# Kernel optimization log

Hardware: AMD Instinct MI355X
Metric: run time of the kernel (lower is better)

Reference implementation:

```python
import jax, jax.numpy as jnp
import numpy as np

ROPE_BASE = 10000.0
NEG_INF = -1e30

def _apply_rope(x):
    # x: [B, H, T, D]; interleaved-pair RoPE (torchtune style), positions along axis -2.
    B, H, T, D = x.shape
    inv_freq = 1.0 / (ROPE_BASE ** (jnp.arange(0, D, 2, dtype=jnp.float32) / D))  # [D/2]
    ang = jnp.arange(T, dtype=jnp.float32)[:, None] * inv_freq[None, :]           # [T, D/2]
    cos, sin = jnp.cos(ang), jnp.sin(ang)
    x1, x2 = x[..., 0::2], x[..., 1::2]                                           # [B,H,T,D/2]
    rot = jnp.stack([x1 * cos - x2 * sin, x1 * sin + x2 * cos], axis=-1)          # [B,H,T,D/2,2]
    return rot.reshape(B, H, T, D).astype(x.dtype)

def setup_inputs() -> dict:
    key = jax.random.key(0)
    ks = jax.random.split(key, 5)
    B, T, C = 2, 2048, 1024
    s = 1.0 / np.sqrt(C)
    return {
        "x":  jax.random.normal(ks[0], (B, T, C), jnp.float32),
        "Wq": jax.random.normal(ks[1], (C, C), jnp.float32) * s,
        "bq": jnp.zeros((C,), jnp.float32),
        "Wk": jax.random.normal(ks[2], (C, C), jnp.float32) * s,
        "bk": jnp.zeros((C,), jnp.float32),
        "Wv": jax.random.normal(ks[3], (C, C), jnp.float32) * s,
        "bv": jnp.zeros((C,), jnp.float32),
        "Wo": jax.random.normal(ks[4], (C, C), jnp.float32) * s,
        "bo": jnp.zeros((C,), jnp.float32),
    }

def reference(x, Wq, bq, Wk, bk, Wv, bv, Wo, bo):
    B, T, C = x.shape
    H = 16
    D = C // H
    # QKV projections (torch Linear: x @ W.T + b), split heads -> [B, H, T, D]
    def proj(W, b):
        return (jnp.einsum('btc,oc->bto', x, W) + b).reshape(B, T, H, D).transpose(0, 2, 1, 3)
    q = _apply_rope(proj(Wq, bq))
    k = _apply_rope(proj(Wk, bk))
    v = proj(Wv, bv)
    # Causal scaled dot-product attention
    scale = 1.0 / jnp.sqrt(jnp.asarray(D, x.dtype))
    scores = jnp.einsum('bhqd,bhkd->bhqk', q, k) * scale                          # [B,H,T,T]
    causal = jnp.tril(jnp.ones((T, T), dtype=bool))
    scores = jnp.where(causal, scores, NEG_INF)
    probs = jax.nn.softmax(scores, axis=-1)
    y = jnp.einsum('bhqk,bhkd->bhqd', probs, v)                                   # [B,H,T,D]
    y = y.transpose(0, 2, 1, 3).reshape(B, T, C)
    # Output projection (dropout is identity in eval mode)
    return jnp.einsum('btc,oc->bto', y, Wo) + bo
```

## Files before the change

### kernel.cpp

```cpp
#include <hip/hip_runtime.h>

#define BB 2
#define TT 2048
#define CC 1024
#define HH 16
#define DD 64
#define KDIM 1024
#define MROWS (BB*TT)

typedef __attribute__((ext_vector_type(8))) short  frag_b16;
typedef __attribute__((ext_vector_type(4))) float  f32x4;
typedef __attribute__((ext_vector_type(4))) unsigned short us4;
typedef __attribute__((ext_vector_type(8))) unsigned short us8;
typedef __attribute__((ext_vector_type(4))) _Float16 f16x4;
typedef __attribute__((ext_vector_type(8))) _Float16 f16x8;

#define EXP2F(x) __builtin_amdgcn_exp2f(x)

__device__ __forceinline__ unsigned short f2bf(float f) {
    unsigned int u = __builtin_bit_cast(unsigned int, f);
    u += 0x7FFFu + ((u >> 16) & 1u);
    return (unsigned short)(u >> 16);
}

__device__ __forceinline__ void gl_lds16(const void* g, void* l) {
    __builtin_amdgcn_global_load_lds(
        (const __attribute__((address_space(1))) unsigned int*)g,
        (__attribute__((address_space(3))) unsigned int*)l, 16, 0, 0);
}

__global__ __launch_bounds__(256) void cvt_all(
        const float* __restrict__ x,  const float* __restrict__ w0,
        const float* __restrict__ w1, const float* __restrict__ w2,
        const float* __restrict__ w3, unsigned short* __restrict__ dst) {
    const size_t NX = (size_t)MROWS * CC;
    const size_t NW = (size_t)CC * CC;
    size_t i = ((size_t)blockIdx.x * 256 + threadIdx.x) * 4;
    const float* src; size_t off;
    if (i < NX) { src = x; off = i; }
    else {
        size_t j = i - NX;
        int t = (int)(j >> 20);
        src = (t == 0) ? w0 : (t == 1) ? w1 : (t == 2) ? w2 : w3;
        off = j & (NW - 1);
    }
    float4 f = *reinterpret_cast<const float4*>(src + off);
    us4 o;
    o.x = f2bf(f.x); o.y = f2bf(f.y); o.z = f2bf(f.z); o.w = f2bf(f.w);
    *reinterpret_cast<us4*>(dst + i) = o;
}

__global__ __launch_bounds__(256, 3) void qkv_gemm_rope(
        const unsigned short* __restrict__ X,
        const unsigned short* __restrict__ Wq,
        const unsigned short* __restrict__ Wk,
        const unsigned short* __restrict__ Wv,
        const float* __restrict__ bq, const float* __restrict__ bk,
        const float* __restrict__ bv,
        unsigned short* __restrict__ Qo,
        unsigned short* __restrict__ Ko,
        _Float16* __restrict__ VTo)
{
    const int z = blockIdx.z;
    const unsigned short* W = (z == 0) ? Wq : (z == 1) ? Wk : Wv;
    const float* bias = (z == 0) ? bq : (z == 1) ? bk : bv;

    const int tid = threadIdx.x;
    const int wave = tid >> 6;
    const int lane = tid & 63;
    const int l16 = lane & 15;
    const int quad = lane >> 4;

    const int bx = blockIdx.x * 128;
    const int by = blockIdx.y * 128;
    const int row0 = bx + (wave >> 1) * 64;
    const int col0 = by + (wave & 1) * 64;

    __shared__ __align__(16) char smem[36864];
    unsigned short (*Xa)[32] = (unsigned short(*)[32])smem;
    unsigned short (*Wb)[32] = (unsigned short(*)[32])(smem + 8192);
    _Float16 (*Vl)[64][72] = (_Float16(*)[64][72])smem;

    f32x4 acc[4][4] = {};

    const int c0 = tid, c1 = tid + 256;
    const int r0s = c0 >> 2, o0s = (c0 & 3) * 8;
    const int r1s = c1 >> 2, o1s = (c1 & 3) * 8;

    for (int kk = 0; kk < KDIM; kk += 32) {
        gl_lds16(X + (size_t)(bx + r0s) * KDIM + kk + o0s, (unsigned short*)Xa + c0 * 8);
        gl_lds16(X + (size_t)(bx + r1s) * KDIM + kk + o1s, (unsigned short*)Xa + c1 * 8);
        gl_lds16(W + (size_t)(by + r0s) * KDIM + kk + o0s, (unsigned short*)Wb + c0 * 8);
        gl_lds16(W + (size_t)(by + r1s) * KDIM + kk + o1s, (unsigned short*)Wb + c1 * 8);
        __syncthreads();

        frag_b16 a[4], b[4];
#pragma unroll
        for (int r = 0; r < 4; ++r)
            a[r] = *reinterpret_cast<const frag_b16*>(
                &Xa[(wave >> 1) * 64 + r * 16 + l16][quad * 8]);
#pragma unroll
        for (int c = 0; c < 4; ++c)
            b[c] = *reinterpret_cast<const frag_b16*>(
                &Wb[(wave & 1) * 64 + c * 16 + l16][quad * 8]);
#pragma unroll
        for (int r = 0; r < 4; ++r)
#pragma unroll
            for (int c = 0; c < 4; ++c)
                acc[r][c] = __builtin_amdgcn_mfma_f32_16x16x32_bf16(a[r], b[c], acc[r][c], 0, 0, 0);
        __syncthreads();
    }

    if (z == 2) {
#pragma unroll
        for (int r = 0; r < 4; ++r)
#pragma unroll
            for (int c = 0; c < 4; ++c) {
                f16x4 pk;
#pragma unroll
                for (int g = 0; g < 4; ++g)
                    pk[g] = (_Float16)(acc[r][c][g] + bias[col0 + c * 16 + l16]);
                *reinterpret_cast<f16x4*>(&Vl[wave][c * 16 + l16][r * 16 + quad * 4]) = pk;
            }
        const int b_ = row0 >> 11;
        const int t_base = row0 & (TT - 1);
        const int h = col0 >> 6;
        const int dl = lane >> 3;
        const int t8 = (lane & 7) * 8;
        __builtin_amdgcn_s_waitcnt(0);
#pragma unroll
        for (int i = 0; i < 8; ++i) {
            int d = i * 8 + dl;
            f16x8 v = *reinterpret_cast<const f16x8*>(&Vl[wave][d][t8]);
            *reinterpret_cast<f16x8*>(
                &VTo[((size_t)(b_ * HH + h) * DD + d) * TT + t_base + t8]) = v;
        }
    } else {
        const float qsc = (z == 0) ? 0.180336888f : 1.0f;
        unsigned short* dst = (z == 0) ? Qo : Ko;
        const int b_ = row0 >> 11;
        const int tq0 = (row0 & (TT - 1)) + quad * 4;
#pragma unroll
        for (int c = 0; c < 4; ++c) {
            const int o = col0 + c * 16 + l16;
            const int h = o >> 6, d = o & (DD - 1);
            const float inv = __expf(-(float)(d & ~1) * (9.210340371976184f / (float)DD));
            float cs0, sn0, cs1, sn1, cs16, sn16;
            __sincosf((float)tq0 * inv, &sn0, &cs0);
            __sincosf(inv, &sn1, &cs1);
            __sincosf(16.f * inv, &sn16, &cs16);
            float cr = cs0, sr = sn0;
#pragma unroll
            for (int r = 0; r < 4; ++r) {
                float cg = cr, sg = sr;
#pragma unroll
                for (int g = 0; g < 4; ++g) {
                    int n = row0 + r * 16 + quad * 4 + g;
                    int t = n & (TT - 1);
                    float v = acc[r][c][g] + bias[o];
                    float pv = __shfl_xor(v, 1);
                    float outv = (d & 1) ? (pv * sg + v * cg) : (v * cg - pv * sg);
                    dst[((size_t)(b_ * HH + h) * TT + t) * DD + d] = f2bf(outv * qsc);
                    float cn = cg * cs1 - sg * sn1;
                    sg = sg * cs1 + cg * sn1;
                    cg = cn;
                }
                float crn = cr * cs16 - sr * sn16;
                sr = sr * cs16 + cr * sn16;
                cr = crn;
            }
        }
    }
}

__global__ __launch_bounds__(256, 2) void attn(
        const unsigned short* __restrict__ Q,
        const unsigned short* __restrict__ K,
        const _Float16* __restrict__ VT,
        unsigned short* __restrict__ Y)
{
    const int b1d = blockIdx.x;
    const int bh = (b1d & 7) * 4 + ((b1d >> 3) & 3);
    const int pair = b1d >> 5;
    const int tid = threadIdx.x;
    const int w = tid >> 6;
    const int lane = tid & 63;
    const int l16 = lane & 15;
    const int quad = lane >> 4;

    const unsigned short* Qp = Q + (size_t)bh * TT * DD;
    const unsigned short* Kp = K + (size_t)bh * TT * DD;
    const _Float16* Vp = VT + (size_t)bh * DD * TT;

    __shared__ unsigned short Kl[2][128][64];
    __shared__ _Float16 Vl[2][64][128];
    __shared__ unsigned short Ylds[4][16][72];

    const int sw = (l16 & 7);
    const int b_ = bh >> 4, h = bh & (HH - 1);

#pragma unroll 1
    for (int seg = 0; seg < 2; ++seg) {
        const int qblk = seg ? (31 - pair) : pair;
        const int q0 = qblk * 64;
        const int q = q0 + w * 16 + l16;

        frag_b16 bq[2];
#pragma unroll
        for (int dk = 0; dk < 2; ++dk)
            bq[dk] = *reinterpret_cast<const frag_b16*>(
                Qp + (size_t)q * DD + dk * 32 + quad * 8);

        f32x4 yacc[4] = {};
        float m = -INFINITY, l = 0.f;

        const int ntiles = (qblk >> 1) + 1;

#pragma unroll
        for (int i = 0; i < 4; ++i) {
            int n = tid + 256 * i;
            int kr = n >> 3,  kc = ((n & 7)  ^ (kr & 7)) * 8;
            int vr = n >> 4,  vc = ((n & 15) ^ (vr & 7)) * 8;
            gl_lds16(Kp + (size_t)kr * DD + kc, (unsigned short*)&Kl[0][0][0] + n * 8);
            gl_lds16(Vp + (size_t)vr * TT + vc, (_Float16*)&Vl[0][0][0] + n * 8);
        }

#pragma unroll 1
        for (int it = 0; it < ntiles; ++it) {
            __syncthreads();
            const int bsel = it & 1;
            if (it + 1 < ntiles) {
                const int jn = (it + 1) * 128;
                const int bn = bsel ^ 1;
#pragma unroll
                for (int i = 0; i < 4; ++i) {
                    int n = tid + 256 * i;
                    int kr = n >> 3,  kc = ((n & 7)  ^ (kr & 7)) * 8;
                    int vr = n >> 4,  vc = ((n & 15) ^ (vr & 7)) * 8;
                    gl_lds16(Kp + (size_t)(jn + kr) * DD + kc,
                             (unsigned short*)&Kl[bn][0][0] + n * 8);
                    gl_lds16(Vp + (size_t)vr * TT + jn + vc,
                             (_Float16*)&Vl[bn][0][0] + n * 8);
                }
            }
            const int j0 = it * 128;

            f32x4 s[8];
#pragma unroll
            for (int mt = 0; mt < 8; ++mt) {
                frag_b16 ak0 = *reinterpret_cast<const frag_b16*>(
                    &Kl[bsel][mt * 16 + l16][(quad ^ sw) * 8]);
                frag_b16 ak1 = *reinterpret_cast<const frag_b16*>(
                    &Kl[bsel][mt * 16 + l16][((4 + quad) ^ sw) * 8]);
                f32x4 t = {};
                t = __builtin_amdgcn_mfma_f32_16x16x32_bf16(ak0, bq[0], t, 0, 0, 0);
                t = __builtin_amdgcn_mfma_f32_16x16x32_bf16(ak1, bq[1], t, 0, 0, 0);
                s[mt] = t;
            }

            float nm = -INFINITY;
            if (it == ntiles - 1) {
#pragma unroll
                for (int mt = 0; mt < 8; ++mt)
#pragma unroll
                    for (int g = 0; g < 4; ++g) {
                        int key = j0 + mt * 16 + quad * 4 + g;
                        float v = s[mt][g];
                        if (key > q) v = -1e30f;
                        s[mt][g] = v;
                        nm = fmaxf(nm, v);
                    }
            } else {
#pragma unroll
                for (int mt = 0; mt < 8; ++mt)
#pragma unroll
                    for (int g = 0; g < 4; ++g)
                        nm = fmaxf(nm, s[mt][g]);
            }
            nm = fmaxf(nm, __shfl_xor(nm, 16));
            nm = fmaxf(nm, __shfl_xor(nm, 32));

            float mn = fmaxf(m, nm);
            float alpha = EXP2F(m - mn);
            m = mn;

            float rs = 0.f;
            f16x4 pb[8];
#pragma unroll
            for (int mt = 0; mt < 8; ++mt)
#pragma unroll
                for (int g = 0; g < 4; ++g) {
                    float e = EXP2F(s[mt][g] - m);
                    pb[mt][g] = (_Float16)e;
                    rs += e;
                }
            rs += __shfl_xor(rs, 16);
            rs += __shfl_xor(rs, 32);
            l = l * alpha + rs;

#pragma unroll
            for (int dt = 0; dt < 4; ++dt) {
                f32x4 ya = yacc[dt];
#pragma unroll
                for (int g = 0; g < 4; ++g) ya[g] *= alpha;
#pragma unroll
                for (int kt = 0; kt < 8; ++kt) {
                    int colp = (kt * 2 + (quad >> 1)) ^ sw;
                    f16x4 av = *reinterpret_cast<const f16x4*>(
                        &Vl[bsel][dt * 16 + l16][colp * 8 + (quad & 1) * 4]);
                    ya = __builtin_amdgcn_mfma_f32_16x16x16f16(av, pb[kt], ya, 0, 0, 0);
                }
                yacc[dt] = ya;
            }
        }

        __syncthreads();

        float rl = 1.f / l;
#pragma unroll
        for (int dt = 0; dt < 4; ++dt)
#pragma unroll
            for (int g = 0; g < 4; ++g)
                Ylds[w][l16][dt * 16 + quad * 4 + g] = f2bf(yacc[dt][g] * rl);

#pragma unroll
        for (int i = 0; i < 2; ++i) {
            int idx = i * 64 + lane;
            int r = idx >> 3, c8 = (idx & 7) * 8;
            us8 v = *reinterpret_cast<const us8*>(&Ylds[w][r][c8]);
            *reinterpret_cast<us8*>(
                &Y[(size_t)(b_ * TT + q0 + w * 16 + r) * CC + h * DD + c8]) = v;
        }
    }
}

__global__ __launch_bounds__(256, 2) void out_gemm(
        const unsigned short* __restrict__ Y,
        const unsigned short* __restrict__ Wo,
        const float* __restrict__ bo,
        float* __restrict__ out)
{
    const int tid = threadIdx.x;
    const int wave = tid >> 6;
    const int lane = tid & 63;
    const int l16 = lane & 15;
    const int quad = lane >> 4;

    const int bx = blockIdx.x * 128;
    const int by = blockIdx.y * 128;
    const int row0 = bx + (wave >> 1) * 64;
    const int col0 = by + (wave & 1) * 64;

    __shared__ unsigned short Xa[128][32];
    __shared__ unsigned short Wb[128][32];

    f32x4 acc[4][4] = {};

    const int c0 = tid, c1 = tid + 256;
    const int r0s = c0 >> 2, o0s = (c0 & 3) * 8;
    const int r1s = c1 >> 2, o1s = (c1 & 3) * 8;

    for (int kk = 0; kk < KDIM; kk += 32) {
        gl_lds16(Y  + (size_t)(bx + r0s) * KDIM + kk + o0s, (unsigned short*)Xa + c0 * 8);
        gl_lds16(Y  + (size_t)(bx + r1s) * KDIM + kk + o1s, (unsigned short*)Xa + c1 * 8);
        gl_lds16(Wo + (size_t)(by + r0s) * KDIM + kk + o0s, (unsigned short*)Wb + c0 * 8);
        gl_lds16(Wo + (size_t)(by + r1s) * KDIM + kk + o1s, (unsigned short*)Wb + c1 * 8);
        __syncthreads();

        frag_b16 a[4], b[4];
#pragma unroll
        for (int r = 0; r < 4; ++r)
            a[r] = *reinterpret_cast<const frag_b16*>(
                &Xa[(wave >> 1) * 64 + r * 16 + l16][quad * 8]);
#pragma unroll
        for (int c = 0; c < 4; ++c)
            b[c] = *reinterpret_cast<const frag_b16*>(
                &Wb[(wave & 1) * 64 + c * 16 + l16][quad * 8]);
#pragma unroll
        for (int r = 0; r < 4; ++r)
#pragma unroll
            for (int c = 0; c < 4; ++c)
                acc[r][c] = __builtin_amdgcn_mfma_f32_16x16x32_bf16(a[r], b[c], acc[r][c], 0, 0, 0);
        __syncthreads();
    }

#pragma unroll
    for (int r = 0; r < 4; ++r)
#pragma unroll
        for (int c = 0; c < 4; ++c)
#pragma unroll
            for (int g = 0; g < 4; ++g) {
                int n = row0 + r * 16 + quad * 4 + g;
                int o = col0 + c * 16 + l16;
                out[(size_t)n * CC + o] = acc[r][c][g] + bo[o];
            }
}

extern "C" void kernel_launch(void* const* d_in, const int* in_sizes, int n_in,
                              void* d_out, int out_size, void* d_ws, size_t ws_size,
                              hipStream_t stream) {
    const float* x  = (const float*)d_in[0];
    const float* Wq = (const float*)d_in[1];
    const float* bq = (const float*)d_in[2];
    const float* Wk = (const float*)d_in[3];
    const float* bk = (const float*)d_in[4];
    const float* Wv = (const float*)d_in[5];
    const float* bv = (const float*)d_in[6];
    const float* Wo = (const float*)d_in[7];
    const float* bo = (const float*)d_in[8];
    float* out = (float*)d_out;

    unsigned short* ws = (unsigned short*)d_ws;
    const size_t NX = (size_t)MROWS * CC;
    const size_t NW = (size_t)CC * CC;
    unsigned short* xb  = ws;
    unsigned short* wqb = xb  + NX;
    unsigned short* wkb = wqb + NW;
    unsigned short* wvb = wkb + NW;
    unsigned short* wob = wvb + NW;
    unsigned short* Qr  = wob + NW;
    unsigned short* Kr  = Qr  + NX;
    _Float16*       VTb = (_Float16*)(Kr + NX);
    unsigned short* Yb  = (unsigned short*)(VTb + NX);

    const size_t NALL = NX + 4 * NW;
    cvt_all<<<dim3((unsigned)(NALL / 1024)), 256, 0, stream>>>(x, Wq, Wk, Wv, Wo, xb);

    qkv_gemm_rope<<<dim3(MROWS / 128, CC / 128, 3), 256, 0, stream>>>(
        xb, wqb, wkb, wvb, bq, bk, bv, Qr, Kr, VTb);

    attn<<<dim3(512), 256, 0, stream>>>(Qr, Kr, VTb, Yb);

    out_gemm<<<dim3(MROWS / 128, CC / 128), 256, 0, stream>>>(Yb, wob, bo, out);
}
```

Before: 183.5 us.

## Process 32 query rows per wave in attention to reuse K/V tiles

```diff
diff --git a/kernel.cpp b/kernel.cpp
--- a/kernel.cpp
+++ b/kernel.cpp
@@ -173,7 +173,7 @@
     }
 }
 
-__global__ __launch_bounds__(256, 2) void attn(
+__global__ __launch_bounds__(256, 1) void attn(
         const unsigned short* __restrict__ Q,
         const unsigned short* __restrict__ K,
         const _Float16* __restrict__ VT,
@@ -194,27 +194,29 @@
 
     __shared__ unsigned short Kl[2][128][64];
     __shared__ _Float16 Vl[2][64][128];
-    __shared__ unsigned short Ylds[4][16][72];
+    __shared__ unsigned short Ylds[4][32][72];
 
     const int sw = (l16 & 7);
     const int b_ = bh >> 4, h = bh & (HH - 1);
 
 #pragma unroll 1
     for (int seg = 0; seg < 2; ++seg) {
-        const int qblk = seg ? (31 - pair) : pair;
-        const int q0 = qblk * 64;
-        const int q = q0 + w * 16 + l16;
-
-        frag_b16 bq[2];
-#pragma unroll
-        for (int dk = 0; dk < 2; ++dk)
-            bq[dk] = *reinterpret_cast<const frag_b16*>(
-                Qp + (size_t)q * DD + dk * 32 + quad * 8);
-
-        f32x4 yacc[4] = {};
-        float m = -INFINITY, l = 0.f;
-
-        const int ntiles = (qblk >> 1) + 1;
+        const int qblk = seg ? (15 - pair) : pair;
+        const int q0 = qblk * 128;
+        const int qw = q0 + w * 32;
+
+        frag_b16 bq[2][2];
+#pragma unroll
+        for (int nt = 0; nt < 2; ++nt)
+#pragma unroll
+            for (int dk = 0; dk < 2; ++dk)
+                bq[nt][dk] = *reinterpret_cast<const frag_b16*>(
+                    Qp + (size_t)(qw + nt * 16 + l16) * DD + dk * 32 + quad * 8);
+
+        f32x4 yacc[2][4] = {};
+        float m[2] = { -INFINITY, -INFINITY }, l[2] = { 0.f, 0.f };
+
+        const int ntiles = qblk + 1;
 
 #pragma unroll
         for (int i = 0; i < 4; ++i) {
@@ -245,91 +247,121 @@
             }
             const int j0 = it * 128;
 
-            f32x4 s[8];
+            f32x4 s[2][8];
 #pragma unroll
             for (int mt = 0; mt < 8; ++mt) {
                 frag_b16 ak0 = *reinterpret_cast<const frag_b16*>(
                     &Kl[bsel][mt * 16 + l16][(quad ^ sw) * 8]);
                 frag_b16 ak1 = *reinterpret_cast<const frag_b16*>(
                     &Kl[bsel][mt * 16 + l16][((4 + quad) ^ sw) * 8]);
-                f32x4 t = {};
-                t = __builtin_amdgcn_mfma_f32_16x16x32_bf16(ak0, bq[0], t, 0, 0, 0);
-                t = __builtin_amdgcn_mfma_f32_16x16x32_bf16(ak1, bq[1], t, 0, 0, 0);
-                s[mt] = t;
-            }
-
-            float nm = -INFINITY;
-            if (it == ntiles - 1) {
+#pragma unroll
+                for (int nt = 0; nt < 2; ++nt) {
+                    f32x4 t = {};
+                    t = __builtin_amdgcn_mfma_f32_16x16x32_bf16(ak0, bq[nt][0], t, 0, 0, 0);
+                    t = __builtin_amdgcn_mfma_f32_16x16x32_bf16(ak1, bq[nt][1], t, 0, 0, 0);
+                    s[nt][mt] = t;
+                }
+            }
+
+            float nm[2] = { -INFINITY, -INFINITY };
+            if (it == qblk) {
+#pragma unroll
+                for (int nt = 0; nt < 2; ++nt) {
+                    const int q = qw + nt * 16 + l16;
+#pragma unroll
+                    for (int mt = 0; mt < 8; ++mt)
+#pragma unroll
+                        for (int g = 0; g < 4; ++g) {
+                            int key = j0 + mt * 16 + quad * 4 + g;
+                            float v = s[nt][mt][g];
+                            if (key > q) v = -1e30f;
+                            s[nt][mt][g] = v;
+                            nm[nt] = fmaxf(nm[nt], v);
+                        }
+                }
+            } else {
+#pragma unroll
+                for (int nt = 0; nt < 2; ++nt)
+#pragma unroll
+                    for (int mt = 0; mt < 8; ++mt)
+#pragma unroll
+                        for (int g = 0; g < 4; ++g)
+                            nm[nt] = fmaxf(nm[nt], s[nt][mt][g]);
+            }
+#pragma unroll
+            for (int nt = 0; nt < 2; ++nt) {
+                nm[nt] = fmaxf(nm[nt], __shfl_xor(nm[nt], 16));
+                nm[nt] = fmaxf(nm[nt], __shfl_xor(nm[nt], 32));
+            }
+
+            float alpha[2];
+#pragma unroll
+            for (int nt = 0; nt < 2; ++nt) {
+                float mn = fmaxf(m[nt], nm[nt]);
+                alpha[nt] = EXP2F(m[nt] - mn);
+                m[nt] = mn;
+            }
+
+            float rs[2] = { 0.f, 0.f };
+            f16x4 pb[2][8];
+#pragma unroll
+            for (int nt = 0; nt < 2; ++nt)
 #pragma unroll
                 for (int mt = 0; mt < 8; ++mt)
 #pragma unroll
                     for (int g = 0; g < 4; ++g) {
-                        int key = j0 + mt * 16 + quad * 4 + g;
-                        float v = s[mt][g];
-                        if (key > q) v = -1e30f;
-                        s[mt][g] = v;
-                        nm = fmaxf(nm, v);
+                        float e = EXP2F(s[nt][mt][g] - m[nt]);
+                        pb[nt][mt][g] = (_Float16)e;
+                        rs[nt] += e;
                     }
-            } else {
-#pragma unroll
-                for (int mt = 0; mt < 8; ++mt)
-#pragma unroll
-                    for (int g = 0; g < 4; ++g)
-                        nm = fmaxf(nm, s[mt][g]);
-            }
-            nm = fmaxf(nm, __shfl_xor(nm, 16));
-            nm = fmaxf(nm, __shfl_xor(nm, 32));
-
-            float mn = fmaxf(m, nm);
-            float alpha = EXP2F(m - mn);
-            m = mn;
-
-            float rs = 0.f;
-            f16x4 pb[8];
-#pragma unroll
-            for (int mt = 0; mt < 8; ++mt)
-#pragma unroll
-                for (int g = 0; g < 4; ++g) {
-                    float e = EXP2F(s[mt][g] - m);
-                    pb[mt][g] = (_Float16)e;
-                    rs += e;
-                }
-            rs += __shfl_xor(rs, 16);
-            rs += __shfl_xor(rs, 32);
-            l = l * alpha + rs;
-
-#pragma unroll
-            for (int dt = 0; dt < 4; ++dt) {
-                f32x4 ya = yacc[dt];
-#pragma unroll
-                for (int g = 0; g < 4; ++g) ya[g] *= alpha;
+#pragma unroll
+            for (int nt = 0; nt < 2; ++nt) {
+                rs[nt] += __shfl_xor(rs[nt], 16);
+                rs[nt] += __shfl_xor(rs[nt], 32);
+                l[nt] = l[nt] * alpha[nt] + rs[nt];
+            }
+
+#pragma unroll
+            for (int nt = 0; nt < 2; ++nt)
+#pragma unroll
+                for (int dt = 0; dt < 4; ++dt)
+#pragma unroll
+                    for (int g = 0; g < 4; ++g) yacc[nt][dt][g] *= alpha[nt];
+#pragma unroll
+            for (int dt = 0; dt < 4; ++dt)
 #pragma unroll
                 for (int kt = 0; kt < 8; ++kt) {
                     int colp = (kt * 2 + (quad >> 1)) ^ sw;
                     f16x4 av = *reinterpret_cast<const f16x4*>(
                         &Vl[bsel][dt * 16 + l16][colp * 8 + (quad & 1) * 4]);
-                    ya = __builtin_amdgcn_mfma_f32_16x16x16f16(av, pb[kt], ya, 0, 0, 0);
+#pragma unroll
+                    for (int nt = 0; nt < 2; ++nt)
+                        yacc[nt][dt] = __builtin_amdgcn_mfma_f32_16x16x16f16(
+                            av, pb[nt][kt], yacc[nt][dt], 0, 0, 0);
                 }
-                yacc[dt] = ya;
-            }
         }
 
         __syncthreads();
 
-        float rl = 1.f / l;
-#pragma unroll
-        for (int dt = 0; dt < 4; ++dt)
-#pragma unroll
-            for (int g = 0; g < 4; ++g)
-                Ylds[w][l16][dt * 16 + quad * 4 + g] = f2bf(yacc[dt][g] * rl);
-
-#pragma unroll
-        for (int i = 0; i < 2; ++i) {
+        float rl[2];
+#pragma unroll
+        for (int nt = 0; nt < 2; ++nt) rl[nt] = 1.f / l[nt];
+#pragma unroll
+        for (int nt = 0; nt < 2; ++nt)
+#pragma unroll
+            for (int dt = 0; dt < 4; ++dt)
+#pragma unroll
+                for (int g = 0; g < 4; ++g)
+                    Ylds[w][nt * 16 + l16][dt * 16 + quad * 4 + g] =
+                        f2bf(yacc[nt][dt][g] * rl[nt]);
+
+#pragma unroll
+        for (int i = 0; i < 4; ++i) {
             int idx = i * 64 + lane;
             int r = idx >> 3, c8 = (idx & 7) * 8;
             us8 v = *reinterpret_cast<const us8*>(&Ylds[w][r][c8]);
             *reinterpret_cast<us8*>(
-                &Y[(size_t)(b_ * TT + q0 + w * 16 + r) * CC + h * DD + c8]) = v;
+                &Y[(size_t)(b_ * TT + q0 + w * 32 + r) * CC + h * DD + c8]) = v;
         }
     }
 }
@@ -429,7 +461,7 @@
     qkv_gemm_rope<<<dim3(MROWS / 128, CC / 128, 3), 256, 0, stream>>>(
         xb, wqb, wkb, wvb, bq, bk, bv, Qr, Kr, VTb);
 
-    attn<<<dim3(512), 256, 0, stream>>>(Qr, Kr, VTb, Yb);
+    attn<<<dim3(256), 256, 0, stream>>>(Qr, Kr, VTb, Yb);
 
     out_gemm<<<dim3(MROWS / 128, CC / 128), 256, 0, stream>>>(Yb, wob, bo, out);
 }
```

Measured after the change: 188.8 us. 1.03x slower.
